# Performance work log

Hardware: AMD Instinct MI355X
Metric: run time of the kernel (lower is better)

## Reference

```python
import jax, jax.numpy as jnp
import numpy as np

C_QKV = 128
C_HID = 32
N_HEADS = 4
INF = 1e9


def setup_inputs() -> dict:
    key = jax.random.key(0)
    ks = jax.random.split(key, 8)
    B, S = 256, 256
    hc = N_HEADS * C_HID  # 128
    inp = {
        "input_qkv": jax.random.normal(ks[0], (1, B, S, C_QKV), dtype=jnp.float32),
        "mask": jnp.ones((1, B, 1, 1, S), dtype=jnp.float32),
        "bias": jax.random.normal(ks[1], (1, 1, N_HEADS, S, S), dtype=jnp.float32),
        "add_transposed_output_to": jax.random.normal(ks[2], (1, B, S, C_QKV), dtype=jnp.float32),
        # linear_qkvg: Linear(c_qkv, 4*h*c), bias=False -> weight [4*hc, c_qkv]
        "W_qkvg": jax.random.normal(ks[3], (4 * hc, C_QKV), dtype=jnp.float32) * (1.0 / np.sqrt(C_QKV)),
        # gating bias initialized to ones in the module
        "linear_g_bias": jnp.ones((hc,), dtype=jnp.float32),
        # linear_o: Linear(hc, c_qkv), init='final' (zeros in AF2, use small random for a nontrivial test)
        "W_o": jax.random.normal(ks[4], (C_QKV, hc), dtype=jnp.float32) * (1.0 / np.sqrt(hc)),
        "b_o": jax.random.normal(ks[5], (C_QKV,), dtype=jnp.float32) * 0.02,
    }
    return inp


def reference(input_qkv, mask, bias, add_transposed_output_to, W_qkvg, linear_g_bias, W_o, b_o):
    hc = N_HEADS * C_HID
    # fused QKVG projection: [1, b, s, 4*hc]
    qkvg = jnp.einsum("xbsc,fc->xbsf", input_qkv, W_qkvg)
    q, k, v, g = jnp.split(qkvg, 4, axis=-1)
    # reshape to heads: [1, b, s, h, c]
    shp = q.shape[:-1] + (N_HEADS, C_HID)
    q = q.reshape(shp)
    k = k.reshape(shp)
    v = v.reshape(shp)
    scale = 1.0 / np.sqrt(C_HID)
    # scores: [1, b, h, q, k]
    a = jnp.einsum("xbqhc,xbkhc->xbhqk", q * scale, k)
    a = a + (mask - 1.0) * INF + bias
    a = jax.nn.softmax(a, axis=-1)
    # attention output: [1, b, q, h, c] -> [1, b, s, hc]
    o = jnp.einsum("xbhqk,xbkhc->xbqhc", a, v)
    o = o.reshape(o.shape[:-2] + (hc,))
    # sigmoid gating
    o = o * jax.nn.sigmoid(g + linear_g_bias)
    # fused linear + transpose(-2,-3) + add
    proj = jnp.einsum("xbsf,of->xbso", o, W_o) + b_o  # [1, b, s, c_qkv]
    out = add_transposed_output_to + jnp.swapaxes(proj, -2, -3)  # [1, s, b, c_qkv]
    return out
```

## Files before the change

kernel.cpp:

```cpp
#include <hip/hip_runtime.h>
#include <math.h>

#define BB 256
#define SS 256
#define NH 4

typedef __attribute__((ext_vector_type(8))) short bfrag;
typedef __attribute__((ext_vector_type(4))) float ffrag;

__device__ inline unsigned short f2bf(float x) {
    unsigned u = __float_as_uint(x);
    u += 0x7FFF + ((u >> 16) & 1);
    return (unsigned short)(u >> 16);
}
__device__ inline float bf2f(unsigned short h) {
    return __uint_as_float(((unsigned)h) << 16);
}
__device__ inline unsigned pack2(float a, float b) {
    return (unsigned)f2bf(a) | ((unsigned)f2bf(b) << 16);
}
union FragU { unsigned u[4]; bfrag b; };

#define XB_OFF  0
#define WB_OFF  8388608
#define WOB_OFF 8454144
#define OG_OFF  8470528

__global__ __launch_bounds__(256) void k0_cast(
    const float* __restrict__ X, const float* __restrict__ W,
    const float* __restrict__ Wo, unsigned short* __restrict__ dst)
{
    const int gid = blockIdx.x * 256 + threadIdx.x;
    const int XN8 = 8388608 / 8, WN8 = 65536 / 8, WoN8 = 16384 / 8;
    const float* src;
    size_t soff, doff;
    if (gid < XN8)            { src = X;  soff = (size_t)gid * 8;                 doff = XB_OFF + soff; }
    else if (gid < XN8 + WN8) { src = W;  soff = (size_t)(gid - XN8) * 8;         doff = WB_OFF + soff; }
    else if (gid < XN8 + WN8 + WoN8) { src = Wo; soff = (size_t)(gid - XN8 - WN8) * 8; doff = WOB_OFF + soff; }
    else return;
    const float4 a = *(const float4*)(src + soff);
    const float4 b = *(const float4*)(src + soff + 4);
    unsigned r0 = pack2(a.x, a.y), r1 = pack2(a.z, a.w);
    unsigned r2 = pack2(b.x, b.y), r3 = pack2(b.z, b.w);
    uint4 o; o.x = r0; o.y = r1; o.z = r2; o.w = r3;
    *(uint4*)(dst + doff) = o;
}

__global__ __launch_bounds__(256, 2) void k_fused(
    const unsigned short* __restrict__ Xb,
    const unsigned short* __restrict__ Wb,
    const float* __restrict__ gbias,
    const float* __restrict__ mask,
    const float* __restrict__ bias,
    unsigned short* __restrict__ og)
{
    const int h = blockIdx.x, b = blockIdx.y;
    const int t = threadIdx.x;
    const int w = t >> 6, lane = t & 63, l15 = lane & 15, quad = lane >> 4;

    __shared__ unsigned short Qb[SS * 40];
    __shared__ unsigned short Kb[SS * 40];
    __shared__ unsigned short Vt[32 * 264];
    __shared__ unsigned short Gb[SS * 34];
    __shared__ float maskLds[SS];

    maskLds[t] = (mask[b * SS + t] - 1.0f) * 1e9f;

    const float qscale = 0.17677669529663687f;

    for (int half = 0; half < 2; ++half) {
        bfrag Wfr[4][4];
#pragma unroll
        for (int f4 = 0; f4 < 4; ++f4) {
            const int floc = (half * 4 + f4) * 16 + l15;
            const int grow = (floc >> 5) * 128 + h * 32 + (floc & 31);
#pragma unroll
            for (int cc = 0; cc < 4; ++cc)
                Wfr[f4][cc] = *(const bfrag*)(Wb + grow * 128 + cc * 32 + quad * 8);
        }
#pragma unroll
        for (int st = 0; st < 4; ++st) {
            const int s = w * 64 + st * 16 + l15;
            bfrag Xfr[4];
#pragma unroll
            for (int cc = 0; cc < 4; ++cc)
                Xfr[cc] = *(const bfrag*)(Xb + (b * SS + s) * 128 + cc * 32 + quad * 8);
#pragma unroll
            for (int f4 = 0; f4 < 4; ++f4) {
                ffrag D = {0.f, 0.f, 0.f, 0.f};
#pragma unroll
                for (int cc = 0; cc < 4; ++cc)
                    D = __builtin_amdgcn_mfma_f32_16x16x32_bf16(Xfr[cc], Wfr[f4][cc], D, 0, 0, 0);
                const int ft = half * 4 + f4;
                const int fcol = ft * 16 + l15;
                const int srow0 = w * 64 + st * 16 + quad * 4;
                if (ft < 2) {
#pragma unroll
                    for (int r = 0; r < 4; ++r)
                        Qb[(srow0 + r) * 40 + fcol] = f2bf(D[r] * qscale);
                } else if (ft < 4) {
#pragma unroll
                    for (int r = 0; r < 4; ++r)
                        Kb[(srow0 + r) * 40 + (fcol - 32)] = f2bf(D[r]);
                } else if (ft < 6) {
                    const int base = (fcol - 64) * 264 + srow0;
                    *(unsigned*)&Vt[base]     = pack2(D[0], D[1]);
                    *(unsigned*)&Vt[base + 2] = pack2(D[2], D[3]);
                } else {
                    const int c = fcol - 96;
                    const float gb = gbias[h * 32 + c];
#pragma unroll
                    for (int r = 0; r < 4; ++r) {
                        const float g = 1.0f / (1.0f + __expf(-(D[r] + gb)));
                        Gb[(srow0 + r) * 34 + c] = f2bf(g);
                    }
                }
            }
        }
    }
    __syncthreads();

    bfrag Vfr[2][8];
#pragma unroll
    for (int ch = 0; ch < 2; ++ch)
#pragma unroll
        for (int ck = 0; ck < 8; ++ck)
            Vfr[ch][ck] = *(const bfrag*)&Vt[(ch * 16 + l15) * 264 + ck * 32 + quad * 8];

    const int srcA = l15 + ((quad & 1) * 2) * 16;
    const int srcB = srcA + 16;
    const bool hi = (quad >> 1) != 0;

    for (int qq = 0; qq < 4; ++qq) {
        const int q = w * 64 + qq * 16 + l15;
        const bfrag Qfr = *(const bfrag*)&Qb[q * 40 + quad * 8];

        ffrag S[16];
#pragma unroll
        for (int kt = 0; kt < 16; ++kt) {
            const bfrag Kfr = *(const bfrag*)&Kb[(kt * 16 + l15) * 40 + quad * 8];
            const ffrag z = {0.f, 0.f, 0.f, 0.f};
            S[kt] = __builtin_amdgcn_mfma_f32_16x16x32_bf16(Kfr, Qfr, z, 0, 0, 0);
        }

        const float* brow = bias + (h * SS + q) * SS;
        float m = -1e30f;
#pragma unroll
        for (int kt = 0; kt < 16; ++kt) {
            const float4 bv = *(const float4*)(brow + kt * 16 + quad * 4);
            const float4 mv = *(const float4*)(maskLds + kt * 16 + quad * 4);
            S[kt][0] += bv.x + mv.x; S[kt][1] += bv.y + mv.y;
            S[kt][2] += bv.z + mv.z; S[kt][3] += bv.w + mv.w;
            m = fmaxf(m, fmaxf(fmaxf(S[kt][0], S[kt][1]), fmaxf(S[kt][2], S[kt][3])));
        }
        m = fmaxf(m, __shfl_xor(m, 16, 64));
        m = fmaxf(m, __shfl_xor(m, 32, 64));

        float l = 0.f;
        unsigned pk[16][2];
#pragma unroll
        for (int kt = 0; kt < 16; ++kt) {
            const float p0 = __expf(S[kt][0] - m);
            const float p1 = __expf(S[kt][1] - m);
            const float p2 = __expf(S[kt][2] - m);
            const float p3 = __expf(S[kt][3] - m);
            l += (p0 + p1) + (p2 + p3);
            pk[kt][0] = pack2(p0, p1);
            pk[kt][1] = pack2(p2, p3);
        }
        l += __shfl_xor(l, 16, 64);
        l += __shfl_xor(l, 32, 64);

        ffrag O[2];
        O[0] = (ffrag){0.f, 0.f, 0.f, 0.f};
        O[1] = (ffrag){0.f, 0.f, 0.f, 0.f};
#pragma unroll
        for (int ck = 0; ck < 8; ++ck) {
            const unsigned a0 = (unsigned)__shfl((int)pk[2 * ck][0],     srcA, 64);
            const unsigned b0 = (unsigned)__shfl((int)pk[2 * ck + 1][0], srcA, 64);
            const unsigned a1 = (unsigned)__shfl((int)pk[2 * ck][1],     srcA, 64);
            const unsigned b1 = (unsigned)__shfl((int)pk[2 * ck + 1][1], srcA, 64);
            const unsigned a2 = (unsigned)__shfl((int)pk[2 * ck][0],     srcB, 64);
            const unsigned b2 = (unsigned)__shfl((int)pk[2 * ck + 1][0], srcB, 64);
            const unsigned a3 = (unsigned)__shfl((int)pk[2 * ck][1],     srcB, 64);
            const unsigned b3 = (unsigned)__shfl((int)pk[2 * ck + 1][1], srcB, 64);
            FragU fu;
            fu.u[0] = hi ? b0 : a0;
            fu.u[1] = hi ? b1 : a1;
            fu.u[2] = hi ? b2 : a2;
            fu.u[3] = hi ? b3 : a3;
            O[0] = __builtin_amdgcn_mfma_f32_16x16x32_bf16(Vfr[0][ck], fu.b, O[0], 0, 0, 0);
            O[1] = __builtin_amdgcn_mfma_f32_16x16x32_bf16(Vfr[1][ck], fu.b, O[1], 0, 0, 0);
        }

        const float invl = 1.0f / l;
        const unsigned short* gr = &Gb[q * 34];
        unsigned* orow = (unsigned*)(og + (b * SS + q) * 128 + h * 32);
#pragma unroll
        for (int ch = 0; ch < 2; ++ch) {
            const int c0 = ch * 16 + quad * 4;
            const float v0 = O[ch][0] * invl * bf2f(gr[c0 + 0]);
            const float v1 = O[ch][1] * invl * bf2f(gr[c0 + 1]);
            const float v2 = O[ch][2] * invl * bf2f(gr[c0 + 2]);
            const float v3 = O[ch][3] * invl * bf2f(gr[c0 + 3]);
            orow[(c0 >> 1) + 0] = pack2(v0, v1);
            orow[(c0 >> 1) + 1] = pack2(v2, v3);
        }
    }
}

__global__ __launch_bounds__(256, 2) void k3_proj(
    const unsigned short* __restrict__ ogb,
    const unsigned short* __restrict__ Wob,
    const float* __restrict__ bo,
    const float* __restrict__ addt,
    float* __restrict__ out)
{
    const int i = blockIdx.x, jh = blockIdx.y;
    const int t = threadIdx.x;
    const int w = t >> 6, lane = t & 63, l15 = lane & 15, quad = lane >> 4;

    __shared__ unsigned short OgS[128 * 136];

    {
        const int jj = t >> 1, hf = t & 1;
        const unsigned short* src = ogb + (((size_t)(jh * 128 + jj) * SS + i) * 128) + hf * 64;
        unsigned short* dst = &OgS[jj * 136 + hf * 64];
#pragma unroll
        for (int u = 0; u < 8; ++u)
            *(uint4*)(dst + u * 8) = *(const uint4*)(src + u * 8);
    }

    bfrag Wfr[2][4];
#pragma unroll
    for (int ctl = 0; ctl < 2; ++ctl) {
        const int crow = (w * 2 + ctl) * 16 + l15;
#pragma unroll
        for (int cc = 0; cc < 4; ++cc)
            Wfr[ctl][cc] = *(const bfrag*)(Wob + crow * 128 + cc * 32 + quad * 8);
    }
    const float bo0 = bo[(w * 2 + 0) * 16 + l15];
    const float bo1 = bo[(w * 2 + 1) * 16 + l15];

    __syncthreads();

#pragma unroll
    for (int jt = 0; jt < 8; ++jt) {
        bfrag Ab[4];
#pragma unroll
        for (int cc = 0; cc < 4; ++cc)
            Ab[cc] = *(const bfrag*)&OgS[(jt * 16 + l15) * 136 + cc * 32 + quad * 8];

        ffrag D0 = {0.f, 0.f, 0.f, 0.f};
        ffrag D1 = {0.f, 0.f, 0.f, 0.f};
#pragma unroll
        for (int cc = 0; cc < 4; ++cc) {
            D0 = __builtin_amdgcn_mfma_f32_16x16x32_bf16(Ab[cc], Wfr[0][cc], D0, 0, 0, 0);
            D1 = __builtin_amdgcn_mfma_f32_16x16x32_bf16(Ab[cc], Wfr[1][cc], D1, 0, 0, 0);
        }

        const int c0 = (w * 2 + 0) * 16 + l15;
        const int c1 = (w * 2 + 1) * 16 + l15;
#pragma unroll
        for (int r = 0; r < 4; ++r) {
            const int j = jh * 128 + jt * 16 + quad * 4 + r;
            const size_t row = (size_t)(i * BB + j) * 128;
            out[row + c0] = D0[r] + bo0 + addt[row + c0];
            out[row + c1] = D1[r] + bo1 + addt[row + c1];
        }
    }
}

extern "C" void kernel_launch(void* const* d_in, const int* in_sizes, int n_in,
                              void* d_out, int out_size, void* d_ws, size_t ws_size,
                              hipStream_t stream) {
    const float* X     = (const float*)d_in[0];
    const float* mask  = (const float*)d_in[1];
    const float* bias  = (const float*)d_in[2];
    const float* addt  = (const float*)d_in[3];
    const float* Wqkvg = (const float*)d_in[4];
    const float* gbias = (const float*)d_in[5];
    const float* Wo    = (const float*)d_in[6];
    const float* bo    = (const float*)d_in[7];
    float* out = (float*)d_out;

    unsigned short* ws = (unsigned short*)d_ws;
    unsigned short* Xb  = ws + XB_OFF;
    unsigned short* Wb  = ws + WB_OFF;
    unsigned short* Wob = ws + WOB_OFF;
    unsigned short* og  = ws + OG_OFF;

    k0_cast<<<4136, 256, 0, stream>>>(X, Wqkvg, Wo, ws);
    k_fused<<<dim3(NH, BB), 256, 0, stream>>>(Xb, Wb, gbias, mask, bias, og);
    k3_proj<<<dim3(SS, 2), 256, 0, stream>>>(og, Wob, bo, addt, out);
}
```

Measured before the change: 234.3 us.

## Software-pipeline softmax of next query tile with PV matmul of previous tile

Restructures the per-warp query-tile loop into a fully unrolled five-step software pipeline. Each step computes QK scores and softmax for tile qq while running the PV MFMA and gated output store for tile qq-1. Packed probabilities and row sums are double-buffered in registers so the scheduler can interleave exp/VALU work with MFMA and shuffles. The extra live registers (a second 32-word pk buffer) could push register pressure past the 2-blocks-per-SM launch bound and cause spills.

```diff
diff --git a/kernel.cpp b/kernel.cpp
--- a/kernel.cpp
+++ b/kernel.cpp
@@ -131,80 +131,94 @@
     const int srcB = srcA + 16;
     const bool hi = (quad >> 1) != 0;
 
-    for (int qq = 0; qq < 4; ++qq) {
-        const int q = w * 64 + qq * 16 + l15;
-        const bfrag Qfr = *(const bfrag*)&Qb[q * 40 + quad * 8];
-
-        ffrag S[16];
-#pragma unroll
-        for (int kt = 0; kt < 16; ++kt) {
-            const bfrag Kfr = *(const bfrag*)&Kb[(kt * 16 + l15) * 40 + quad * 8];
-            const ffrag z = {0.f, 0.f, 0.f, 0.f};
-            S[kt] = __builtin_amdgcn_mfma_f32_16x16x32_bf16(Kfr, Qfr, z, 0, 0, 0);
-        }
-
-        const float* brow = bias + (h * SS + q) * SS;
-        float m = -1e30f;
-#pragma unroll
-        for (int kt = 0; kt < 16; ++kt) {
-            const float4 bv = *(const float4*)(brow + kt * 16 + quad * 4);
-            const float4 mv = *(const float4*)(maskLds + kt * 16 + quad * 4);
-            S[kt][0] += bv.x + mv.x; S[kt][1] += bv.y + mv.y;
-            S[kt][2] += bv.z + mv.z; S[kt][3] += bv.w + mv.w;
-            m = fmaxf(m, fmaxf(fmaxf(S[kt][0], S[kt][1]), fmaxf(S[kt][2], S[kt][3])));
-        }
-        m = fmaxf(m, __shfl_xor(m, 16, 64));
-        m = fmaxf(m, __shfl_xor(m, 32, 64));
-
-        float l = 0.f;
-        unsigned pk[16][2];
-#pragma unroll
-        for (int kt = 0; kt < 16; ++kt) {
-            const float p0 = __expf(S[kt][0] - m);
-            const float p1 = __expf(S[kt][1] - m);
-            const float p2 = __expf(S[kt][2] - m);
-            const float p3 = __expf(S[kt][3] - m);
-            l += (p0 + p1) + (p2 + p3);
-            pk[kt][0] = pack2(p0, p1);
-            pk[kt][1] = pack2(p2, p3);
-        }
-        l += __shfl_xor(l, 16, 64);
-        l += __shfl_xor(l, 32, 64);
-
-        ffrag O[2];
-        O[0] = (ffrag){0.f, 0.f, 0.f, 0.f};
-        O[1] = (ffrag){0.f, 0.f, 0.f, 0.f};
-#pragma unroll
-        for (int ck = 0; ck < 8; ++ck) {
-            const unsigned a0 = (unsigned)__shfl((int)pk[2 * ck][0],     srcA, 64);
-            const unsigned b0 = (unsigned)__shfl((int)pk[2 * ck + 1][0], srcA, 64);
-            const unsigned a1 = (unsigned)__shfl((int)pk[2 * ck][1],     srcA, 64);
-            const unsigned b1 = (unsigned)__shfl((int)pk[2 * ck + 1][1], srcA, 64);
-            const unsigned a2 = (unsigned)__shfl((int)pk[2 * ck][0],     srcB, 64);
-            const unsigned b2 = (unsigned)__shfl((int)pk[2 * ck + 1][0], srcB, 64);
-            const unsigned a3 = (unsigned)__shfl((int)pk[2 * ck][1],     srcB, 64);
-            const unsigned b3 = (unsigned)__shfl((int)pk[2 * ck + 1][1], srcB, 64);
-            FragU fu;
-            fu.u[0] = hi ? b0 : a0;
-            fu.u[1] = hi ? b1 : a1;
-            fu.u[2] = hi ? b2 : a2;
-            fu.u[3] = hi ? b3 : a3;
-            O[0] = __builtin_amdgcn_mfma_f32_16x16x32_bf16(Vfr[0][ck], fu.b, O[0], 0, 0, 0);
-            O[1] = __builtin_amdgcn_mfma_f32_16x16x32_bf16(Vfr[1][ck], fu.b, O[1], 0, 0, 0);
-        }
-
-        const float invl = 1.0f / l;
-        const unsigned short* gr = &Gb[q * 34];
-        unsigned* orow = (unsigned*)(og + (b * SS + q) * 128 + h * 32);
-#pragma unroll
-        for (int ch = 0; ch < 2; ++ch) {
-            const int c0 = ch * 16 + quad * 4;
-            const float v0 = O[ch][0] * invl * bf2f(gr[c0 + 0]);
-            const float v1 = O[ch][1] * invl * bf2f(gr[c0 + 1]);
-            const float v2 = O[ch][2] * invl * bf2f(gr[c0 + 2]);
-            const float v3 = O[ch][3] * invl * bf2f(gr[c0 + 3]);
-            orow[(c0 >> 1) + 0] = pack2(v0, v1);
-            orow[(c0 >> 1) + 1] = pack2(v2, v3);
+    unsigned pk[2][16][2];
+    float lbuf[2];
+
+#pragma unroll
+    for (int step = 0; step < 5; ++step) {
+        if (step < 4) {
+            const int qq = step;
+            const int cur = qq & 1;
+            const int q = w * 64 + qq * 16 + l15;
+            const bfrag Qfr = *(const bfrag*)&Qb[q * 40 + quad * 8];
+
+            ffrag S[16];
+#pragma unroll
+            for (int kt = 0; kt < 16; ++kt) {
+                const bfrag Kfr = *(const bfrag*)&Kb[(kt * 16 + l15) * 40 + quad * 8];
+                const ffrag z = {0.f, 0.f, 0.f, 0.f};
+                S[kt] = __builtin_amdgcn_mfma_f32_16x16x32_bf16(Kfr, Qfr, z, 0, 0, 0);
+            }
+
+            const float* brow = bias + (h * SS + q) * SS;
+            float m = -1e30f;
+#pragma unroll
+            for (int kt = 0; kt < 16; ++kt) {
+                const float4 bv = *(const float4*)(brow + kt * 16 + quad * 4);
+                const float4 mv = *(const float4*)(maskLds + kt * 16 + quad * 4);
+                S[kt][0] += bv.x + mv.x; S[kt][1] += bv.y + mv.y;
+                S[kt][2] += bv.z + mv.z; S[kt][3] += bv.w + mv.w;
+                m = fmaxf(m, fmaxf(fmaxf(S[kt][0], S[kt][1]), fmaxf(S[kt][2], S[kt][3])));
+            }
+            m = fmaxf(m, __shfl_xor(m, 16, 64));
+            m = fmaxf(m, __shfl_xor(m, 32, 64));
+
+            float l = 0.f;
+#pragma unroll
+            for (int kt = 0; kt < 16; ++kt) {
+                const float p0 = __expf(S[kt][0] - m);
+                const float p1 = __expf(S[kt][1] - m);
+                const float p2 = __expf(S[kt][2] - m);
+                const float p3 = __expf(S[kt][3] - m);
+                l += (p0 + p1) + (p2 + p3);
+                pk[cur][kt][0] = pack2(p0, p1);
+                pk[cur][kt][1] = pack2(p2, p3);
+            }
+            l += __shfl_xor(l, 16, 64);
+            l += __shfl_xor(l, 32, 64);
+            lbuf[cur] = l;
+        }
+
+        if (step > 0) {
+            const int qq = step - 1;
+            const int prv = qq & 1;
+            const int q = w * 64 + qq * 16 + l15;
+
+            ffrag O[2];
+            O[0] = (ffrag){0.f, 0.f, 0.f, 0.f};
+            O[1] = (ffrag){0.f, 0.f, 0.f, 0.f};
+#pragma unroll
+            for (int ck = 0; ck < 8; ++ck) {
+                const unsigned a0 = (unsigned)__shfl((int)pk[prv][2 * ck][0],     srcA, 64);
+                const unsigned b0 = (unsigned)__shfl((int)pk[prv][2 * ck + 1][0], srcA, 64);
+                const unsigned a1 = (unsigned)__shfl((int)pk[prv][2 * ck][1],     srcA, 64);
+                const unsigned b1 = (unsigned)__shfl((int)pk[prv][2 * ck + 1][1], srcA, 64);
+                const unsigned a2 = (unsigned)__shfl((int)pk[prv][2 * ck][0],     srcB, 64);
+                const unsigned b2 = (unsigned)__shfl((int)pk[prv][2 * ck + 1][0], srcB, 64);
+                const unsigned a3 = (unsigned)__shfl((int)pk[prv][2 * ck][1],     srcB, 64);
+                const unsigned b3 = (unsigned)__shfl((int)pk[prv][2 * ck + 1][1], srcB, 64);
+                FragU fu;
+                fu.u[0] = hi ? b0 : a0;
+                fu.u[1] = hi ? b1 : a1;
+                fu.u[2] = hi ? b2 : a2;
+                fu.u[3] = hi ? b3 : a3;
+                O[0] = __builtin_amdgcn_mfma_f32_16x16x32_bf16(Vfr[0][ck], fu.b, O[0], 0, 0, 0);
+                O[1] = __builtin_amdgcn_mfma_f32_16x16x32_bf16(Vfr[1][ck], fu.b, O[1], 0, 0, 0);
+            }
+
+            const float invl = 1.0f / lbuf[prv];
+            const unsigned short* gr = &Gb[q * 34];
+            unsigned* orow = (unsigned*)(og + (b * SS + q) * 128 + h * 32);
+#pragma unroll
+            for (int ch = 0; ch < 2; ++ch) {
+                const int c0 = ch * 16 + quad * 4;
+                const float v0 = O[ch][0] * invl * bf2f(gr[c0 + 0]);
+                const float v1 = O[ch][1] * invl * bf2f(gr[c0 + 1]);
+                const float v2 = O[ch][2] * invl * bf2f(gr[c0 + 2]);
+                const float v3 = O[ch][3] * invl * bf2f(gr[c0 + 3]);
+                orow[(c0 >> 1) + 0] = pack2(v0, v1);
+                orow[(c0 >> 1) + 1] = pack2(v2, v3);
+            }
         }
     }
 }
```

New measurement: 259.8 us. 1.11x slower.
